# Kernel optimization log

Measured on AMD Instinct MI355X. Metric: run time of the kernel, lower is better.

## Reference

```python
import jax, jax.numpy as jnp
import numpy as np

NEG_SLOPE = 0.2
EPS = 1e-16


def gat_conv(x, src, dst, W, a_src, a_dst, b, num_nodes):
    # Single-head PyG GATConv (heads=1, add_self_loops already applied via src/dst).
    h = x @ W                                   # [N, C]
    alpha_s = h @ a_src                         # [N]
    alpha_d = h @ a_dst                         # [N]
    e = jax.nn.leaky_relu(alpha_s[src] + alpha_d[dst], NEG_SLOPE)  # [E]
    # softmax over incoming edges per destination node
    m = jax.ops.segment_max(e, dst, num_segments=num_nodes)        # [N]
    ex = jnp.exp(e - m[dst])
    denom = jax.ops.segment_sum(ex, dst, num_segments=num_nodes)   # [N]
    alpha = ex / (denom[dst] + EPS)                                 # [E]
    out = jax.ops.segment_sum(h[src] * alpha[:, None], dst, num_segments=num_nodes)
    return out + b


def setup_inputs() -> dict:
    key = jax.random.key(0)
    ks = jax.random.split(key, 10)
    N, E, F_in, H, C = 100000, 1600000, 64, 64, 32
    x = jax.random.normal(ks[0], (N, F_in), dtype=jnp.float32)
    edge_index = jax.random.randint(ks[1], (2, E), 0, N, dtype=jnp.int64)
    s1 = 1.0 / np.sqrt(F_in)
    s2 = 1.0 / np.sqrt(H)
    return {
        "x": x,
        "edge_index": edge_index,
        "W1": jax.random.normal(ks[2], (F_in, H), dtype=jnp.float32) * s1,
        "a1_src": jax.random.normal(ks[3], (H,), dtype=jnp.float32) * s2,
        "a1_dst": jax.random.normal(ks[4], (H,), dtype=jnp.float32) * s2,
        "b1": jnp.zeros((H,), dtype=jnp.float32),
        "W2": jax.random.normal(ks[5], (H, C), dtype=jnp.float32) * s2,
        "a2_src": jax.random.normal(ks[6], (C,), dtype=jnp.float32) / np.sqrt(C),
        "a2_dst": jax.random.normal(ks[7], (C,), dtype=jnp.float32) / np.sqrt(C),
        "b2": jnp.zeros((C,), dtype=jnp.float32),
    }


def reference(x, edge_index, W1, a1_src, a1_dst, b1, W2, a2_src, a2_dst, b2):
    N = x.shape[0]
    loops = jnp.arange(N, dtype=edge_index.dtype)
    src = jnp.concatenate([edge_index[0], loops])  # add self-loops (GATConv default)
    dst = jnp.concatenate([edge_index[1], loops])
    # dropout layers are no-ops in eval mode
    h = jax.nn.relu(gat_conv(x, src, dst, W1, a1_src, a1_dst, b1, N))
    out = gat_conv(h, src, dst, W2, a2_src, a2_dst, b2, N)
    return jax.nn.log_softmax(out, axis=-1)
```

## Files before the change

### kernel.cpp

```cpp
#include <hip/hip_runtime.h>

typedef unsigned int uint;
typedef unsigned short ushort;
typedef short short8 __attribute__((ext_vector_type(8)));
typedef float floatx4 __attribute__((ext_vector_type(4)));

#define LEAKY(e) ((e) > 0.f ? (e) : 0.2f * (e))
#define BCAP 1536
#define NBMAX 2048
#define EPT 32
#define TILE (256 * EPT)

__device__ __forceinline__ ushort f2bf(float f) {
    uint u = __float_as_uint(f);
    return (ushort)((u + 0x7fffu + ((u >> 16) & 1u)) >> 16);
}
__device__ __forceinline__ float bflo(uint u) { return __uint_as_float(u << 16); }
__device__ __forceinline__ float bfhi(uint u) { return __uint_as_float(u & 0xffff0000u); }

__device__ __forceinline__ void binK_body(
    int bid, const int* __restrict__ srcA, const int* __restrict__ dstA,
    int* __restrict__ bcur, int* __restrict__ binned, int E, int Etot, int nbuck)
{
    __shared__ int hist[NBMAX];
    __shared__ int basep[NBMAX];
    int t = threadIdx.x;
    long long start = (long long)bid * TILE;

    for (int i = t; i < NBMAX; i += 256) hist[i] = 0;
    __syncthreads();

    short bs[EPT];
    int vals[EPT];
#pragma unroll
    for (int j = 0; j < EPT; ++j) {
        long long i = start + (long long)j * 256 + t;
        if (i < Etot) {
            int s, d;
            if (i < E) { s = srcA[i]; d = dstA[i]; } else { s = d = (int)(i - E); }
            int b = d >> 6;
            bs[j] = (short)b;
            vals[j] = (s << 6) | (d & 63);
            atomicAdd(&hist[b], 1);
        } else bs[j] = -1;
    }
    __syncthreads();

    for (int b = t; b < nbuck; b += 256) {
        int hc = hist[b];
        basep[b] = hc ? atomicAdd(bcur + b * 16, hc) : 0;
    }
    __syncthreads();
    for (int i = t; i < NBMAX; i += 256) hist[i] = 0;
    __syncthreads();

#pragma unroll
    for (int j = 0; j < EPT; ++j) {
        int b = bs[j];
        if (b >= 0) {
            int pos = basep[b] + atomicAdd(&hist[b], 1);
            if (pos < BCAP) binned[(size_t)b * BCAP + pos] = vals[j];
        }
    }
}

__device__ __forceinline__ void gemm1_body(
    int bid, const float* __restrict__ x, const float* __restrict__ W,
    const float* __restrict__ a_src, const float* __restrict__ a_dst,
    ushort* __restrict__ hb, float* __restrict__ as, float* __restrict__ ad, int N)
{
    int tid = threadIdx.x;
    int wave = tid >> 6, lane = tid & 63;
    int q = lane >> 4, c0 = lane & 15;
    int rowbase = bid * 64 + wave * 16;
    int arow = rowbase + c0;
    bool aok = arow < N;

    short8 afrag[2];
#pragma unroll
    for (int kb = 0; kb < 2; ++kb) {
        float xa[8];
        if (aok) {
            const float4 u0 = *(const float4*)(x + (size_t)arow * 64 + kb * 32 + q * 8);
            const float4 u1 = *(const float4*)(x + (size_t)arow * 64 + kb * 32 + q * 8 + 4);
            xa[0] = u0.x; xa[1] = u0.y; xa[2] = u0.z; xa[3] = u0.w;
            xa[4] = u1.x; xa[5] = u1.y; xa[6] = u1.z; xa[7] = u1.w;
        } else {
#pragma unroll
            for (int j = 0; j < 8; ++j) xa[j] = 0.f;
        }
#pragma unroll
        for (int j = 0; j < 8; ++j) afrag[kb][j] = (short)f2bf(xa[j]);
    }

    short8 bfrag[4][2];
#pragma unroll
    for (int t = 0; t < 4; ++t)
#pragma unroll
        for (int kb = 0; kb < 2; ++kb)
#pragma unroll
            for (int j = 0; j < 8; ++j)
                bfrag[t][kb][j] = (short)f2bf(W[(size_t)(kb * 32 + q * 8 + j) * 64 + t * 16 + c0]);

    floatx4 acc[4];
#pragma unroll
    for (int t = 0; t < 4; ++t) acc[t] = (floatx4){0.f, 0.f, 0.f, 0.f};
#pragma unroll
    for (int t = 0; t < 4; ++t)
#pragma unroll
        for (int kb = 0; kb < 2; ++kb)
            acc[t] = __builtin_amdgcn_mfma_f32_16x16x32_bf16(afrag[kb], bfrag[t][kb], acc[t], 0, 0, 0);

    float a_s[4], a_d[4];
#pragma unroll
    for (int t = 0; t < 4; ++t) { a_s[t] = a_src[t * 16 + c0]; a_d[t] = a_dst[t * 16 + c0]; }
    float vs[4], vd[4];
#pragma unroll
    for (int r = 0; r < 4; ++r) {
        vs[r] = 0.f; vd[r] = 0.f;
#pragma unroll
        for (int t = 0; t < 4; ++t) { vs[r] += acc[t][r] * a_s[t]; vd[r] += acc[t][r] * a_d[t]; }
    }
#pragma unroll
    for (int o = 1; o < 16; o <<= 1)
#pragma unroll
        for (int r = 0; r < 4; ++r) {
            vs[r] += __shfl_xor(vs[r], o, 16);
            vd[r] += __shfl_xor(vd[r], o, 16);
        }
    int drow = rowbase + q * 4;
    if (c0 == 0) {
#pragma unroll
        for (int r = 0; r < 4; ++r)
            if (drow + r < N) { as[drow + r] = vs[r]; ad[drow + r] = vd[r]; }
    }
#pragma unroll
    for (int r = 0; r < 4; ++r) {
        if (drow + r < N) {
#pragma unroll
            for (int t = 0; t < 4; ++t)
                hb[(size_t)(drow + r) * 64 + t * 16 + c0] = f2bf(acc[t][r]);
        }
    }
}

__global__ __launch_bounds__(256) void fusedK(
    const int* __restrict__ srcA, const int* __restrict__ dstA,
    int* __restrict__ bcur, int* __restrict__ binned, int E, int Etot, int nbuck, int tb,
    const float* __restrict__ x, const float* __restrict__ W,
    const float* __restrict__ a_src, const float* __restrict__ a_dst,
    ushort* __restrict__ hb, float* __restrict__ as, float* __restrict__ ad, int N)
{
    int b = (int)blockIdx.x;
    if (b < tb) binK_body(b, srcA, dstA, bcur, binned, E, Etot, nbuck);
    else gemm1_body(b - tb, x, W, a_src, a_dst, hb, as, ad, N);
}

__global__ __launch_bounds__(512) void bagg1gemm2K(
    const int* __restrict__ bcur, const int* __restrict__ binned,
    int* __restrict__ csr, int* __restrict__ off, int* __restrict__ deg_out,
    const float* __restrict__ as, const float* __restrict__ ad,
    const ushort* __restrict__ hb1, const float* __restrict__ b1,
    const float* __restrict__ W,
    const float* __restrict__ a_src, const float* __restrict__ a_dst,
    ushort* __restrict__ hb2, float* __restrict__ as2, float* __restrict__ ad2, int N)
{
    __shared__ int histL[64];
    __shared__ int offL[64];
    __shared__ int curL[64];
    __shared__ int csrL[BCAP];
    __shared__ float aggL[64 * 68];
    int b = blockIdx.x;
    int t = threadIdx.x;
    int cnt = min(bcur[b * 16], BCAP);
    const int* bin = binned + (size_t)b * BCAP;

    if (t < 64) histL[t] = 0;
    __syncthreads();
    for (int i = t; i < cnt; i += 512) atomicAdd(&histL[bin[i] & 63], 1);
    __syncthreads();
    if (t < 64) {
        int v = histL[t];
        int x = v;
#pragma unroll
        for (int o = 1; o < 64; o <<= 1) {
            int y = __shfl_up(x, o, 64);
            if (t >= o) x += y;
        }
        int excl = x - v;
        offL[t] = excl;
        curL[t] = excl;
        int d = b * 64 + t;
        if (d < N) { off[d] = b * BCAP + excl; deg_out[d] = v; }
    }
    __syncthreads();
    for (int i = t; i < cnt; i += 512) {
        int e = bin[i];
        int p = atomicAdd(&curL[e & 63], 1);
        int s = e >> 6;
        csrL[p] = s;
        csr[(size_t)b * BCAP + p] = s;
    }
    __syncthreads();

    int lid = t & 7;
    int nl = t >> 3;
    int n = b * 64 + nl;

    float den = 0.f;
    float acc[8];
#pragma unroll
    for (int k = 0; k < 8; ++k) acc[k] = 0.f;

    if (n < N) {
        int p0 = offL[nl];
        int pend = p0 + histL[nl];
        float adn = ad[n];
        int base = p0;
        for (; base + 8 <= pend; base += 8) {
            int s_l = csrL[base + lid];
            float a_l = as[s_l];
            uint4 v[8];
#pragma unroll
            for (int j = 0; j < 8; ++j) {
                int s_j = __shfl(s_l, j, 8);
                v[j] = *(const uint4*)(hb1 + (size_t)s_j * 64 + lid * 8);
            }
            float w_l = __expf(LEAKY(a_l + adn));
            den += w_l;
#pragma unroll
            for (int j = 0; j < 8; ++j) {
                float w = __shfl(w_l, j, 8);
                acc[0] += w * bflo(v[j].x); acc[1] += w * bfhi(v[j].x);
                acc[2] += w * bflo(v[j].y); acc[3] += w * bfhi(v[j].y);
                acc[4] += w * bflo(v[j].z); acc[5] += w * bfhi(v[j].z);
                acc[6] += w * bflo(v[j].w); acc[7] += w * bfhi(v[j].w);
            }
        }
        int r = pend - base;
        if (r) {
            int s_l = 0; float w_l = 0.f;
            if (lid < r) { s_l = csrL[base + lid]; w_l = __expf(LEAKY(as[s_l] + adn)); }
            den += w_l;
#pragma unroll
            for (int j = 0; j < 8; ++j) {
                if (j < r) {
                    int s_j = __shfl(s_l, j, 8);
                    float w = __shfl(w_l, j, 8);
                    const uint4 v = *(const uint4*)(hb1 + (size_t)s_j * 64 + lid * 8);
                    acc[0] += w * bflo(v.x); acc[1] += w * bfhi(v.x);
                    acc[2] += w * bflo(v.y); acc[3] += w * bfhi(v.y);
                    acc[4] += w * bflo(v.z); acc[5] += w * bfhi(v.z);
                    acc[6] += w * bflo(v.w); acc[7] += w * bfhi(v.w);
                }
            }
        }
#pragma unroll
        for (int o = 4; o > 0; o >>= 1) den += __shfl_xor(den, o, 8);
    } else den = 1.f;

    float inv = 1.f / den;
    float4 o0 = make_float4(acc[0] * inv, acc[1] * inv, acc[2] * inv, acc[3] * inv);
    float4 o1 = make_float4(acc[4] * inv, acc[5] * inv, acc[6] * inv, acc[7] * inv);
    *(float4*)&aggL[nl * 68 + lid * 8] = o0;
    *(float4*)&aggL[nl * 68 + lid * 8 + 4] = o1;
    __syncthreads();

    int wave = t >> 6, lane = t & 63;
    if (wave >= 4) return;
    int q = lane >> 4, m = lane & 15;
    int rowbase = b * 64 + wave * 16;

    short8 afrag[2];
#pragma unroll
    for (int kb = 0; kb < 2; ++kb) {
#pragma unroll
        for (int j = 0; j < 8; ++j) {
            float xv = aggL[(wave * 16 + m) * 68 + kb * 32 + q * 8 + j] + b1[kb * 32 + q * 8 + j];
            afrag[kb][j] = (short)f2bf(xv > 0.f ? xv : 0.f);
        }
    }

    short8 bfrag[2][2];
#pragma unroll
    for (int tt = 0; tt < 2; ++tt)
#pragma unroll
        for (int kb = 0; kb < 2; ++kb)
#pragma unroll
            for (int j = 0; j < 8; ++j)
                bfrag[tt][kb][j] = (short)f2bf(W[(size_t)(kb * 32 + q * 8 + j) * 32 + tt * 16 + m]);

    floatx4 cacc[2];
#pragma unroll
    for (int tt = 0; tt < 2; ++tt) cacc[tt] = (floatx4){0.f, 0.f, 0.f, 0.f};
#pragma unroll
    for (int tt = 0; tt < 2; ++tt)
#pragma unroll
        for (int kb = 0; kb < 2; ++kb)
            cacc[tt] = __builtin_amdgcn_mfma_f32_16x16x32_bf16(afrag[kb], bfrag[tt][kb], cacc[tt], 0, 0, 0);

    float a_s[2], a_d[2];
#pragma unroll
    for (int tt = 0; tt < 2; ++tt) { a_s[tt] = a_src[tt * 16 + m]; a_d[tt] = a_dst[tt * 16 + m]; }
    float vs[4], vd[4];
#pragma unroll
    for (int r = 0; r < 4; ++r) {
        vs[r] = 0.f; vd[r] = 0.f;
#pragma unroll
        for (int tt = 0; tt < 2; ++tt) { vs[r] += cacc[tt][r] * a_s[tt]; vd[r] += cacc[tt][r] * a_d[tt]; }
    }
#pragma unroll
    for (int o = 1; o < 16; o <<= 1)
#pragma unroll
        for (int r = 0; r < 4; ++r) {
            vs[r] += __shfl_xor(vs[r], o, 16);
            vd[r] += __shfl_xor(vd[r], o, 16);
        }
    int drow = rowbase + q * 4;
    if (m == 0) {
#pragma unroll
        for (int r = 0; r < 4; ++r)
            if (drow + r < N) { as2[drow + r] = vs[r]; ad2[drow + r] = vd[r]; }
    }
#pragma unroll
    for (int r = 0; r < 4; ++r) {
        if (drow + r < N) {
#pragma unroll
            for (int tt = 0; tt < 2; ++tt)
                hb2[(size_t)(drow + r) * 32 + tt * 16 + m] = f2bf(cacc[tt][r]);
        }
    }
}

__global__ __launch_bounds__(256) void node_agg2(
    const int* __restrict__ csr_src, const int* __restrict__ off,
    const int* __restrict__ deg,
    const float* __restrict__ as, const float* __restrict__ ad,
    const ushort* __restrict__ hb, const float* __restrict__ b2,
    float* __restrict__ out, int N)
{
    int tid = threadIdx.x;
    int lid = tid & 3;
    int n = blockIdx.x * 64 + (tid >> 2);
    if (n >= N) return;
    int p0 = off[n], p1 = p0 + deg[n];
    float adn = ad[n];

    float den = 0.f;
    float acc[8];
#pragma unroll
    for (int k = 0; k < 8; ++k) acc[k] = 0.f;

    int base = p0;
    for (; base + 4 <= p1; base += 4) {
        int s_l = csr_src[base + lid];
        float a_l = as[s_l];
        uint4 v[4];
#pragma unroll
        for (int j = 0; j < 4; ++j) {
            int s_j = __shfl(s_l, j, 4);
            v[j] = *(const uint4*)(hb + (size_t)s_j * 32 + lid * 8);
        }
        float w_l = __expf(LEAKY(a_l + adn));
        den += w_l;
#pragma unroll
        for (int j = 0; j < 4; ++j) {
            float w = __shfl(w_l, j, 4);
            acc[0] += w * bflo(v[j].x); acc[1] += w * bfhi(v[j].x);
            acc[2] += w * bflo(v[j].y); acc[3] += w * bfhi(v[j].y);
            acc[4] += w * bflo(v[j].z); acc[5] += w * bfhi(v[j].z);
            acc[6] += w * bflo(v[j].w); acc[7] += w * bfhi(v[j].w);
        }
    }
    int r = p1 - base;
    if (r) {
        int s_l = 0; float w_l = 0.f;
        if (lid < r) { s_l = csr_src[base + lid]; w_l = __expf(LEAKY(as[s_l] + adn)); }
        den += w_l;
#pragma unroll
        for (int j = 0; j < 4; ++j) {
            if (j < r) {
                int s_j = __shfl(s_l, j, 4);
                float w = __shfl(w_l, j, 4);
                const uint4 v = *(const uint4*)(hb + (size_t)s_j * 32 + lid * 8);
                acc[0] += w * bflo(v.x); acc[1] += w * bfhi(v.x);
                acc[2] += w * bflo(v.y); acc[3] += w * bfhi(v.y);
                acc[4] += w * bflo(v.z); acc[5] += w * bfhi(v.z);
                acc[6] += w * bflo(v.w); acc[7] += w * bfhi(v.w);
            }
        }
    }
#pragma unroll
    for (int o = 2; o > 0; o >>= 1) den += __shfl_xor(den, o, 4);
    float inv = 1.f / den;
#pragma unroll
    for (int k = 0; k < 8; ++k) acc[k] = acc[k] * inv + b2[lid * 8 + k];

    float mx = acc[0];
#pragma unroll
    for (int k = 1; k < 8; ++k) mx = fmaxf(mx, acc[k]);
#pragma unroll
    for (int o = 2; o > 0; o >>= 1) mx = fmaxf(mx, __shfl_xor(mx, o, 4));
    float se = 0.f;
#pragma unroll
    for (int k = 0; k < 8; ++k) se += __expf(acc[k] - mx);
#pragma unroll
    for (int o = 2; o > 0; o >>= 1) se += __shfl_xor(se, o, 4);
    float lse = mx + __logf(se);
    float4 o0 = make_float4(acc[0] - lse, acc[1] - lse, acc[2] - lse, acc[3] - lse);
    float4 o1 = make_float4(acc[4] - lse, acc[5] - lse, acc[6] - lse, acc[7] - lse);
    float* op = out + (size_t)n * 32 + lid * 8;
    *(float4*)op = o0;
    *(float4*)(op + 4) = o1;
}

extern "C" void kernel_launch(void* const* d_in, const int* in_sizes, int n_in,
                              void* d_out, int out_size, void* d_ws, size_t ws_size,
                              hipStream_t stream) {
    const float* x   = (const float*)d_in[0];
    const int*   ei  = (const int*)d_in[1];
    const float* W1  = (const float*)d_in[2];
    const float* a1s = (const float*)d_in[3];
    const float* a1d = (const float*)d_in[4];
    const float* b1  = (const float*)d_in[5];
    const float* W2  = (const float*)d_in[6];
    const float* a2s = (const float*)d_in[7];
    const float* a2d = (const float*)d_in[8];
    const float* b2  = (const float*)d_in[9];

    int N = in_sizes[0] / 64;
    int E = in_sizes[1] / 2;
    int Etot = E + N;
    int nbuck = (N + 63) >> 6;
    const int* srcA = ei;
    const int* dstA = ei + E;

    float* ws = (float*)d_ws;
    ushort* hb1 = (ushort*)ws;
    ushort* hb2 = hb1 + (size_t)N * 64;
    float* as1  = ws + (size_t)N * 48;
    float* ad1  = as1 + N;
    float* as2  = ad1 + N;
    float* ad2  = as2 + N;
    int* off    = (int*)(ad2 + N);
    int* deg    = off + N;
    int* bcur   = deg + N;
    int* csr    = bcur + (size_t)nbuck * 16;
    int* binned = csr + (size_t)nbuck * BCAP;

    hipMemsetAsync(bcur, 0, sizeof(int) * (size_t)nbuck * 16, stream);

    int tb = (int)(((long long)Etot + TILE - 1) / TILE);
    int g1 = (N + 63) / 64;

    fusedK<<<tb + g1, 256, 0, stream>>>(srcA, dstA, bcur, binned, E, Etot, nbuck, tb,
                                        x, W1, a1s, a1d, hb1, as1, ad1, N);
    bagg1gemm2K<<<nbuck, 512, 0, stream>>>(bcur, binned, csr, off, deg,
                                           as1, ad1, hb1, b1, W2, a2s, a2d,
                                           hb2, as2, ad2, N);
    node_agg2<<<(N + 63) / 64, 256, 0, stream>>>(csr, off, deg, as2, ad2, hb2, b2,
                                                 (float*)d_out, N);
}
```

Measured before the change: 204.0 us.

## Bin edges into 256-node coarse buckets and re-read indices instead of caching

The binning stage now groups edges by dst>>8 into 256-node buckets of capacity 6144, which shrinks the shared histogram to 512 entries and cuts the number of global bucket-cursor atomics. Each aggregation block (64 nodes) scans the whole coarse bucket and keeps only edges whose sub-bucket matches its quarter. The binning kernel also reads dst twice (once for the histogram, once to scatter) instead of holding bucket ids and packed values in registers, which lowers register pressure. The cost is four times as much bucket data scanned in the aggregation kernel and an extra global read of dst and src.

```diff
diff --git a/kernel.cpp b/kernel.cpp
--- a/kernel.cpp
+++ b/kernel.cpp
@@ -6,8 +6,8 @@
 typedef float floatx4 __attribute__((ext_vector_type(4)));
 
 #define LEAKY(e) ((e) > 0.f ? (e) : 0.2f * (e))
-#define BCAP 1536
-#define NBMAX 2048
+#define BCAP256 6144
+#define BCAP64 1536
 #define EPT 32
 #define TILE (256 * EPT)
 
@@ -22,44 +22,41 @@
     int bid, const int* __restrict__ srcA, const int* __restrict__ dstA,
     int* __restrict__ bcur, int* __restrict__ binned, int E, int Etot, int nbuck)
 {
-    __shared__ int hist[NBMAX];
-    __shared__ int basep[NBMAX];
+    __shared__ int hist[512];
+    __shared__ int basep[512];
     int t = threadIdx.x;
     long long start = (long long)bid * TILE;
 
-    for (int i = t; i < NBMAX; i += 256) hist[i] = 0;
-    __syncthreads();
-
-    short bs[EPT];
-    int vals[EPT];
+    hist[t] = 0; hist[t + 256] = 0;
+    __syncthreads();
+
+#pragma unroll
+    for (int j = 0; j < EPT; ++j) {
+        long long i = start + (long long)j * 256 + t;
+        if (i < Etot) {
+            int d = (i < E) ? dstA[i] : (int)(i - E);
+            atomicAdd(&hist[d >> 8], 1);
+        }
+    }
+    __syncthreads();
+
+    for (int b = t; b < nbuck; b += 256) {
+        int hc = hist[b];
+        basep[b] = hc ? atomicAdd(bcur + b * 16, hc) : 0;
+    }
+    __syncthreads();
+    hist[t] = 0; hist[t + 256] = 0;
+    __syncthreads();
+
 #pragma unroll
     for (int j = 0; j < EPT; ++j) {
         long long i = start + (long long)j * 256 + t;
         if (i < Etot) {
             int s, d;
             if (i < E) { s = srcA[i]; d = dstA[i]; } else { s = d = (int)(i - E); }
-            int b = d >> 6;
-            bs[j] = (short)b;
-            vals[j] = (s << 6) | (d & 63);
-            atomicAdd(&hist[b], 1);
-        } else bs[j] = -1;
-    }
-    __syncthreads();
-
-    for (int b = t; b < nbuck; b += 256) {
-        int hc = hist[b];
-        basep[b] = hc ? atomicAdd(bcur + b * 16, hc) : 0;
-    }
-    __syncthreads();
-    for (int i = t; i < NBMAX; i += 256) hist[i] = 0;
-    __syncthreads();
-
-#pragma unroll
-    for (int j = 0; j < EPT; ++j) {
-        int b = bs[j];
-        if (b >= 0) {
+            int b = d >> 8;
             int pos = basep[b] + atomicAdd(&hist[b], 1);
-            if (pos < BCAP) binned[(size_t)b * BCAP + pos] = vals[j];
+            if (pos < BCAP256) binned[(size_t)b * BCAP256 + pos] = (s << 8) | (d & 255);
         }
     }
 }
@@ -168,16 +165,21 @@
     __shared__ int histL[64];
     __shared__ int offL[64];
     __shared__ int curL[64];
-    __shared__ int csrL[BCAP];
+    __shared__ int csrL[BCAP64];
     __shared__ float aggL[64 * 68];
     int b = blockIdx.x;
+    int pb = b >> 2;
+    int qq = b & 3;
     int t = threadIdx.x;
-    int cnt = min(bcur[b * 16], BCAP);
-    const int* bin = binned + (size_t)b * BCAP;
+    int cnt = min(bcur[pb * 16], BCAP256);
+    const int* bin = binned + (size_t)pb * BCAP256;
 
     if (t < 64) histL[t] = 0;
     __syncthreads();
-    for (int i = t; i < cnt; i += 512) atomicAdd(&histL[bin[i] & 63], 1);
+    for (int i = t; i < cnt; i += 512) {
+        int dl = bin[i] & 255;
+        if ((dl >> 6) == qq) atomicAdd(&histL[dl & 63], 1);
+    }
     __syncthreads();
     if (t < 64) {
         int v = histL[t];
@@ -191,15 +193,18 @@
         offL[t] = excl;
         curL[t] = excl;
         int d = b * 64 + t;
-        if (d < N) { off[d] = b * BCAP + excl; deg_out[d] = v; }
+        if (d < N) { off[d] = b * BCAP64 + excl; deg_out[d] = v; }
     }
     __syncthreads();
     for (int i = t; i < cnt; i += 512) {
         int e = bin[i];
-        int p = atomicAdd(&curL[e & 63], 1);
-        int s = e >> 6;
-        csrL[p] = s;
-        csr[(size_t)b * BCAP + p] = s;
+        int dl = e & 255;
+        if ((dl >> 6) == qq) {
+            int p = atomicAdd(&curL[dl & 63], 1);
+            int s = e >> 8;
+            csrL[p] = s;
+            csr[(size_t)b * BCAP64 + p] = s;
+        }
     }
     __syncthreads();
 
@@ -431,7 +436,8 @@
     int N = in_sizes[0] / 64;
     int E = in_sizes[1] / 2;
     int Etot = E + N;
-    int nbuck = (N + 63) >> 6;
+    int nbuck256 = (N + 255) >> 8;
+    int nbuck64  = (N + 63) >> 6;
     const int* srcA = ei;
     const int* dstA = ei + E;
 
@@ -445,19 +451,19 @@
     int* off    = (int*)(ad2 + N);
     int* deg    = off + N;
     int* bcur   = deg + N;
-    int* csr    = bcur + (size_t)nbuck * 16;
-    int* binned = csr + (size_t)nbuck * BCAP;
-
-    hipMemsetAsync(bcur, 0, sizeof(int) * (size_t)nbuck * 16, stream);
+    int* csr    = bcur + (size_t)nbuck256 * 16;
+    int* binned = csr + (size_t)nbuck64 * BCAP64;
+
+    hipMemsetAsync(bcur, 0, sizeof(int) * (size_t)nbuck256 * 16, stream);
 
     int tb = (int)(((long long)Etot + TILE - 1) / TILE);
     int g1 = (N + 63) / 64;
 
-    fusedK<<<tb + g1, 256, 0, stream>>>(srcA, dstA, bcur, binned, E, Etot, nbuck, tb,
+    fusedK<<<tb + g1, 256, 0, stream>>>(srcA, dstA, bcur, binned, E, Etot, nbuck256, tb,
                                         x, W1, a1s, a1d, hb1, as1, ad1, N);
-    bagg1gemm2K<<<nbuck, 512, 0, stream>>>(bcur, binned, csr, off, deg,
-                                           as1, ad1, hb1, b1, W2, a2s, a2d,
-                                           hb2, as2, ad2, N);
+    bagg1gemm2K<<<nbuck64, 512, 0, stream>>>(bcur, binned, csr, off, deg,
+                                             as1, ad1, hb1, b1, W2, a2s, a2d,
+                                             hb2, as2, ad2, N);
     node_agg2<<<(N + 63) / 64, 256, 0, stream>>>(csr, off, deg, as2, ad2, hb2, b2,
                                                  (float*)d_out, N);
 }
```

Measured after the change: 206.3 us. Within noise of the previous version (+1.2%).
